# Kernel tuning notes

Hardware: AMD Instinct MI355X
Metric: run time of the kernel (lower is better)

## Reference

```python
import jax, jax.numpy as jnp
import numpy as np

NUM_HEADS = 16
CHUNK = 512


def setup_inputs() -> dict:
    key = jax.random.key(0)
    k1, k2, k3 = jax.random.split(key, 3)
    B, S, H = 2, 2048, 1024
    x = jax.random.normal(k1, (B, S, H), dtype=jnp.float32)
    w_qkv = jax.random.normal(k2, (H, 3 * H), dtype=jnp.float32) * 0.02
    b_qkv = jnp.zeros((3 * H,), dtype=jnp.float32)
    w_proj = jax.random.normal(k3, (H, H), dtype=jnp.float32) * 0.02
    b_proj = jnp.zeros((H,), dtype=jnp.float32)
    return {"x": x, "w_qkv": w_qkv, "b_qkv": b_qkv, "w_proj": w_proj, "b_proj": b_proj}


def reference(x, w_qkv, b_qkv, w_proj, b_proj):
    B, S, H = x.shape
    nh, cs = NUM_HEADS, CHUNK
    hd = H // nh
    nc = S // cs  # number of chunks (seq_len > chunk_size -> chunked branch)

    qkv = x @ w_qkv + b_qkv  # [B,S,3H]
    qkv = qkv.reshape(B, S, 3, nh, hd).transpose(2, 0, 3, 1, 4)  # [3,B,nh,S,hd]
    q, k, v = qkv[0], qkv[1], qkv[2]  # each [B,nh,S,hd]

    # split sequence into chunks: [B,nh,nc,cs,hd]
    qc = q.reshape(B, nh, nc, cs, hd)
    kc = k.reshape(B, nh, nc, cs, hd)
    vc = v.reshape(B, nh, nc, cs, hd)

    scale = 1.0 / jnp.sqrt(jnp.asarray(hd, dtype=x.dtype))
    # scores for every (q-chunk i, k-chunk j) pair: [B,nh,i,j,cs,cs]
    scores = jnp.einsum('bhicd,bhjed->bhijce', qc, kc) * scale
    # softmax is LOCAL to each k-chunk (per pair), matching the torch code
    attn = jax.nn.softmax(scores, axis=-1)
    # attend within each pair, then AVERAGE over k-chunks j
    out = jnp.einsum('bhijce,bhjed->bhicd', attn, vc) / nc  # [B,nh,nc,cs,hd]

    out = out.reshape(B, nh, S, hd).transpose(0, 2, 1, 3).reshape(B, S, H)
    # dropout is identity in eval mode
    return out @ w_proj + b_proj
```

## Files before the change

kernel.cpp:

```cpp
#include <hip/hip_runtime.h>
#include <hip/hip_bf16.h>
#include <stdint.h>

typedef __bf16 bf16;
typedef __bf16 bf16x8 __attribute__((ext_vector_type(8)));
typedef __bf16 bf16x4 __attribute__((ext_vector_type(4)));
typedef float f32x4 __attribute__((ext_vector_type(4)));

#define MFMA16(a, b, c) __builtin_amdgcn_mfma_f32_16x16x32_bf16(a, b, c, 0, 0, 0)
#define SBAR() __builtin_amdgcn_sched_barrier(0)

__device__ __forceinline__ void gload_lds16(const void* g, void* l) {
  __builtin_amdgcn_global_load_lds(
      (const __attribute__((address_space(1))) void*)g,
      (__attribute__((address_space(3))) void*)l, 16, 0, 0);
}


__global__ void prep_kernel(const float* __restrict__ x, bf16* __restrict__ xb,
                            const float* __restrict__ w_qkv,
                            bf16* __restrict__ wqkvT,
                            const float* __restrict__ w_proj,
                            bf16* __restrict__ wprojT) {
  __shared__ float t[32][65];
  const int bid = blockIdx.x;
  if (bid < 4096) {
    const int i = (bid * 256 + threadIdx.x) * 4;
    const float4 v = *(const float4*)(x + i);
    bf16x4 o = {(bf16)v.x, (bf16)v.y, (bf16)v.z, (bf16)v.w};
    *(bf16x4*)(xb + i) = o;
  } else {
    const float* in;
    bf16* out;
    int C, tile;
    if (bid < 5632) {
      in = w_qkv; out = wqkvT; C = 3072; tile = bid - 4096;
    } else {
      in = w_proj; out = wprojT; C = 1024; tile = bid - 5632;
    }
    const int ntx = C >> 5;
    const int c0 = (tile % ntx) * 32, r0 = (tile / ntx) * 64;
    const int tx = threadIdx.x & 31, ty = threadIdx.x >> 5;
#pragma unroll
    for (int i = 0; i < 64; i += 8)
      t[tx][ty + i] = in[(size_t)(r0 + ty + i) * C + c0 + tx];
    __syncthreads();
    const int orr = threadIdx.x & 63, oc4 = threadIdx.x >> 6;
#pragma unroll
    for (int i = 0; i < 32; i += 4) {
      const int oc = i + oc4;
      out[(size_t)(c0 + oc) * 1024 + r0 + orr] = (bf16)t[oc][orr];
    }
  }
}

__global__ void reduce_ctx(const bf16* __restrict__ p1, bf16* __restrict__ ctx) {
  const int i = (blockIdx.x * blockDim.x + threadIdx.x) * 8;
  const bf16x8 a = *(const bf16x8*)(ctx + i);
  const bf16x8 b = *(const bf16x8*)(p1 + i);
  bf16x8 o;
#pragma unroll
  for (int j = 0; j < 8; ++j)
    o[j] = (bf16)(0.25f * ((float)a[j] + (float)b[j]));
  *(bf16x8*)(ctx + i) = o;
}


__global__ __launch_bounds__(256, 2) void gemm_qkv(
    const bf16* __restrict__ A, const bf16* __restrict__ Bt,
    const float* __restrict__ bias, bf16* __restrict__ qp,
    bf16* __restrict__ kp, bf16* __restrict__ vT) {
  __shared__ __align__(16) char smem[65536];
  const int tid = threadIdx.x;
  const int wid = tid >> 6, lane = tid & 63;
  const int l15 = lane & 15, g = lane >> 4;
  const int wg = (blockIdx.x & 7) * 96 + (blockIdx.x >> 3);
  const int m0 = (wg / 24) * 128, n0 = (wg % 24) * 128;
  const int wr = wid >> 1, wc = wid & 1;
  const int K = 1024, nt = 16;

  const int srow8 = lane >> 3;
  const int sxor = ((lane & 7) ^ srow8) << 3;

  auto stage = [&](int t, int buf) {
    const int kt = t * 64;
    char* bufA = smem + buf * 32768;
    char* bufB = bufA + 16384;
#pragma unroll
    for (int c = 0; c < 4; ++c) {
      const int r = wid * 32 + c * 8 + srow8;
      gload_lds16(A + (size_t)(m0 + r) * K + kt + sxor,
                  bufA + wid * 4096 + c * 1024);
      gload_lds16(Bt + (size_t)(n0 + r) * K + kt + sxor,
                  bufB + wid * 4096 + c * 1024);
    }
  };

  f32x4 acc[4][4] = {};

  stage(0, 0);

  const int rsw = (l15 & 7) << 4;

#pragma unroll 1
  for (int t = 0; t < nt; ++t) {
    __syncthreads();
    SBAR();
    if (t + 1 < nt) stage(t + 1, (t + 1) & 1);
    const char* lA = smem + (t & 1) * 32768;
    const char* lB = lA + 16384;
#pragma unroll
    for (int kk = 0; kk < 2; ++kk) {
      const int kb = kk * 64 + g * 16;
      bf16x8 af[4], bfr[4];
#pragma unroll
      for (int mi = 0; mi < 4; ++mi)
        af[mi] = *(const bf16x8*)(lA + (wr * 64 + mi * 16 + l15) * 128 +
                                  (kb ^ rsw));
#pragma unroll
      for (int ni = 0; ni < 4; ++ni)
        bfr[ni] = *(const bf16x8*)(lB + (wc * 64 + ni * 16 + l15) * 128 +
                                   (kb ^ rsw));
      __builtin_amdgcn_s_setprio(1);
#pragma unroll
      for (int mi = 0; mi < 4; ++mi)
#pragma unroll
        for (int ni = 0; ni < 4; ++ni)
          acc[mi][ni] = MFMA16(af[mi], bfr[ni], acc[mi][ni]);
      __builtin_amdgcn_s_setprio(0);
    }
  }

  __syncthreads();
  const int b = m0 >> 11;
  if (n0 >= 2048) {
    bf16* T = (bf16*)smem + (size_t)wid * (64 * 68);
#pragma unroll
    for (int ni = 0; ni < 4; ++ni) {
      const float bv = bias[n0 + wc * 64 + ni * 16 + l15];
#pragma unroll
      for (int mi = 0; mi < 4; ++mi)
#pragma unroll
        for (int rg = 0; rg < 4; ++rg)
          T[(ni * 16 + l15) * 68 + mi * 16 + g * 4 + rg] =
              (bf16)(acc[mi][ni][rg] + bv);
    }
    const int hh = (n0 - 2048 + wc * 64) >> 6;
    const int sbase = (m0 & 2047) + wr * 64;
    const int l15p = (l15 & 8) | ((l15 & 3) << 1) | ((l15 >> 2) & 1);
    bf16* vrow = vT + ((size_t)(b * 16 + hh) * 64) * 2048 + sbase;
#pragma unroll
    for (int rr = 0; rr < 16; ++rr) {
      const int d = rr * 4 + g;
      const bf16x4 v4 = *(const bf16x4*)(T + d * 68 + l15 * 4);
      *(bf16x4*)(vrow + (size_t)d * 2048 + l15p * 4) = v4;
    }
  } else {
    const int sec = n0 >> 10;
    bf16* dst = (sec == 0) ? qp : kp;
    const float qscale = (sec == 0) ? 0.1803368801f : 1.0f;
#pragma unroll
    for (int mi = 0; mi < 4; ++mi) {
      const int rbase = m0 + wr * 64 + mi * 16 + g * 4;
#pragma unroll
      for (int ni = 0; ni < 4; ++ni) {
        const int cc = n0 + wc * 64 + ni * 16 + l15;
        const float bv = bias[cc];
        const int hh = (cc >> 6) & 15, d = cc & 63;
#pragma unroll
        for (int rg = 0; rg < 4; ++rg) {
          const int r = rbase + rg;
          const int s = r & 2047;
          dst[((size_t)(b * 16 + hh) * 2048 + s) * 64 + d] =
              (bf16)((acc[mi][ni][rg] + bv) * qscale);
        }
      }
    }
  }
}


__global__ __launch_bounds__(256, 2) void gemm_proj(
    const bf16* __restrict__ A, const bf16* __restrict__ Bt,
    const float* __restrict__ bias, float* __restrict__ Cout, int M, int N,
    int K, int nxb) {
  __shared__ __align__(16) char smem[65536];
  const int tid = threadIdx.x;
  const int wid = tid >> 6, lane = tid & 63;
  const int l15 = lane & 15, g = lane >> 4;
  const int cpx = gridDim.x >> 3;
  const int wg = (blockIdx.x & 7) * cpx + (blockIdx.x >> 3);
  const int m0 = (wg / nxb) * 128, n0 = (wg % nxb) * 128;
  const int wr = wid >> 1, wc = wid & 1;
  const int nt = K / 64;

  const int srow8 = lane >> 3;
  const int sxor = ((lane & 7) ^ srow8) << 3;

  auto stage = [&](int t, int buf) {
    const int kt = t * 64;
    char* bufA = smem + buf * 32768;
    char* bufB = bufA + 16384;
#pragma unroll
    for (int c = 0; c < 4; ++c) {
      const int r = wid * 32 + c * 8 + srow8;
      gload_lds16(A + (size_t)(m0 + r) * K + kt + sxor,
                  bufA + wid * 4096 + c * 1024);
      gload_lds16(Bt + (size_t)(n0 + r) * K + kt + sxor,
                  bufB + wid * 4096 + c * 1024);
    }
  };

  f32x4 acc[4][4] = {};

  stage(0, 0);

  const int rsw = (l15 & 7) << 4;

#pragma unroll 1
  for (int t = 0; t < nt; ++t) {
    __syncthreads();
    SBAR();
    if (t + 1 < nt) stage(t + 1, (t + 1) & 1);
    const char* lA = smem + (t & 1) * 32768;
    const char* lB = lA + 16384;
#pragma unroll
    for (int kk = 0; kk < 2; ++kk) {
      const int kb = kk * 64 + g * 16;
      bf16x8 af[4], bfr[4];
#pragma unroll
      for (int mi = 0; mi < 4; ++mi)
        af[mi] = *(const bf16x8*)(lA + (wr * 64 + mi * 16 + l15) * 128 +
                                  (kb ^ rsw));
#pragma unroll
      for (int ni = 0; ni < 4; ++ni)
        bfr[ni] = *(const bf16x8*)(lB + (wc * 64 + ni * 16 + l15) * 128 +
                                   (kb ^ rsw));
      __builtin_amdgcn_s_setprio(1);
#pragma unroll
      for (int mi = 0; mi < 4; ++mi)
#pragma unroll
        for (int ni = 0; ni < 4; ++ni)
          acc[mi][ni] = MFMA16(af[mi], bfr[ni], acc[mi][ni]);
      __builtin_amdgcn_s_setprio(0);
    }
  }

#pragma unroll
  for (int mi = 0; mi < 4; ++mi) {
    const int rbase = m0 + wr * 64 + mi * 16 + g * 4;
#pragma unroll
    for (int ni = 0; ni < 4; ++ni) {
      const int cc = n0 + wc * 64 + ni * 16 + l15;
      const float bv = bias[cc];
#pragma unroll
      for (int rg = 0; rg < 4; ++rg)
        Cout[(size_t)(rbase + rg) * N + cc] = acc[mi][ni][rg] + bv;
    }
  }
}


__global__ __launch_bounds__(256, 4) void attn_kernel(
    const bf16* __restrict__ qp, const bf16* __restrict__ kp,
    const bf16* __restrict__ vT, bf16* __restrict__ p0,
    bf16* __restrict__ p1) {
  __shared__ __align__(16) char lds_raw[32768];

  const int tid = threadIdx.x;
  const int wid = tid >> 6, lane = tid & 63;
  const int l15 = lane & 15, g = lane >> 4;
  const int wg = (blockIdx.x & 7) * 128 + (blockIdx.x >> 3);
  const int ch = wg & 1, qt = (wg >> 1) & 15, bhh = wg >> 5;
  const int h = bhh & 15, b = bhh >> 4;
  const size_t bh = (size_t)bhh;
  const int rowbase = b * 2048 + qt * 128;

  const bf16* qptr = qp + (bh * 2048 + (size_t)qt * 128 + wid * 32) * 64;
  bf16x8 Qf[2][2];
#pragma unroll
  for (int m = 0; m < 2; ++m)
#pragma unroll
    for (int hf = 0; hf < 2; ++hf)
      Qf[m][hf] =
          *(const bf16x8*)(qptr + (size_t)(m * 16 + l15) * 64 + hf * 32 + g * 8);

  bf16x8 ones;
#pragma unroll
  for (int i = 0; i < 8; ++i) ones[i] = (bf16)1.0f;

  const bf16* kbase = kp + bh * 2048 * 64;
  const bf16* vbase = vT + bh * 64 * 2048;

  const int srow = lane >> 3;
  const int scol = 8 * ((lane & 7) ^ srow);
  char* ldsK = lds_raw;
  char* ldsV = lds_raw + 16384;

  auto stage = [&](int tile, int buf) {
    const int r0 = wid * 16 + srow;
    const bf16* ks = kbase + ((size_t)tile * 64 + r0) * 64 + scol;
    char* kd = ldsK + buf * 8192 + wid * 2048;
    gload_lds16(ks, kd);
    gload_lds16(ks + 8 * 64, kd + 1024);
    const bf16* vs = vbase + (size_t)r0 * 2048 + tile * 64 + scol;
    char* vd = ldsV + buf * 8192 + wid * 2048;
    gload_lds16(vs, vd);
    gload_lds16(vs + 8 * 2048, vd + 1024);
  };

  f32x4 Otot[2][4] = {};
  const int swz = (l15 & 7) << 4;

  stage(ch * 16, 0);

#pragma unroll 1
  for (int c2 = 0; c2 < 2; ++c2) {
    f32x4 Och[2][4] = {};
    f32x4 ssum[2] = {};
#pragma unroll 1
    for (int h8 = 0; h8 < 8; ++h8) {
      const int t = c2 * 8 + h8;
      __syncthreads();
      SBAR();
      stage(ch * 16 + ((t + 1) & 15), (t + 1) & 1);
      const char* Kt = ldsK + (t & 1) * 8192;
      const char* Vt = ldsV + (t & 1) * 8192;
#pragma unroll
      for (int kk2 = 0; kk2 < 2; ++kk2) {
        f32x4 sacc[2][2] = {};
        __builtin_amdgcn_s_setprio(1);
#pragma unroll
        for (int b2 = 0; b2 < 2; ++b2)
#pragma unroll
          for (int hf = 0; hf < 2; ++hf) {
            const bf16x8 kf =
                *(const bf16x8*)(Kt + ((kk2 * 2 + b2) * 16 + l15) * 128 +
                                 ((hf * 64 + g * 16) ^ swz));
            sacc[b2][0] = MFMA16(kf, Qf[0][hf], sacc[b2][0]);
            sacc[b2][1] = MFMA16(kf, Qf[1][hf], sacc[b2][1]);
          }
        __builtin_amdgcn_s_setprio(0);
        bf16x8 af[2];
#pragma unroll
        for (int m = 0; m < 2; ++m)
#pragma unroll
          for (int j = 0; j < 4; ++j) {
            af[m][j] = (bf16)__builtin_amdgcn_exp2f(sacc[0][m][j]);
            af[m][4 + j] = (bf16)__builtin_amdgcn_exp2f(sacc[1][m][j]);
          }
        __builtin_amdgcn_s_setprio(1);
#pragma unroll
        for (int n = 0; n < 4; ++n) {
          const bf16x8 vf = *(const bf16x8*)(Vt + (n * 16 + l15) * 128 +
                                             ((kk2 * 64 + g * 16) ^ swz));
          Och[0][n] = MFMA16(af[0], vf, Och[0][n]);
          Och[1][n] = MFMA16(af[1], vf, Och[1][n]);
        }
        ssum[0] = MFMA16(af[0], ones, ssum[0]);
        ssum[1] = MFMA16(af[1], ones, ssum[1]);
        __builtin_amdgcn_s_setprio(0);
      }
    }
#pragma unroll
    for (int m = 0; m < 2; ++m)
#pragma unroll
      for (int rg = 0; rg < 4; ++rg) {
        const float inv = __builtin_amdgcn_rcpf(ssum[m][rg]);
#pragma unroll
        for (int n = 0; n < 4; ++n) Otot[m][n][rg] += Och[m][n][rg] * inv;
      }
  }

  bf16* pc = ch ? p1 : p0;
#pragma unroll
  for (int m = 0; m < 2; ++m)
#pragma unroll
    for (int n = 0; n < 4; ++n)
#pragma unroll
      for (int rg = 0; rg < 4; ++rg) {
        const int r = rowbase + wid * 32 + m * 16 + g * 4 + rg;
        pc[(size_t)r * 1024 + h * 64 + n * 16 + l15] = (bf16)Otot[m][n][rg];
      }
}


extern "C" void kernel_launch(void* const* d_in, const int* in_sizes, int n_in,
                              void* d_out, int out_size, void* d_ws,
                              size_t ws_size, hipStream_t stream) {
  const float* x = (const float*)d_in[0];
  const float* w_qkv = (const float*)d_in[1];
  const float* b_qkv = (const float*)d_in[2];
  const float* w_proj = (const float*)d_in[3];
  const float* b_proj = (const float*)d_in[4];
  float* out = (float*)d_out;

  char* ws = (char*)d_ws;
  bf16* xb     = (bf16*)(ws);
  bf16* wqkvT  = (bf16*)(ws + (8u << 20));
  bf16* wprojT = (bf16*)(ws + (14u << 20));
  bf16* qp     = (bf16*)(ws + (16u << 20));
  bf16* kp     = (bf16*)(ws + (24u << 20));
  bf16* vT     = (bf16*)(ws + (32u << 20));
  bf16* ctx    = (bf16*)(ws + (40u << 20));

  hipLaunchKernelGGL(prep_kernel, dim3(6144), dim3(256), 0, stream, x, xb,
                     w_qkv, wqkvT, w_proj, wprojT);
  hipLaunchKernelGGL(gemm_qkv, dim3(768), dim3(256), 0, stream, xb, wqkvT,
                     b_qkv, qp, kp, vT);
  hipLaunchKernelGGL(attn_kernel, dim3(1024), dim3(256), 0, stream, qp, kp, vT,
                     ctx, xb);
  hipLaunchKernelGGL(reduce_ctx, dim3(2048), dim3(256), 0, stream, xb, ctx);
  hipLaunchKernelGGL(gemm_proj, dim3(8 * 32), dim3(256), 0, stream, ctx,
                     wprojT, b_proj, out, 4096, 1024, 1024, 8);
}
```

Baseline: 99.61 us.

## Triple-buffer A tiles and use partial vmcnt waits in QKV and proj GEMMs

Both GEMM kernels now keep three LDS buffers for the A operand and two for B. A is prefetched two k-steps ahead and B one step ahead. The full __syncthreads is replaced by an explicit s_waitcnt vmcnt(4) plus s_barrier, so the next tile's loads can stay in flight while the current one is consumed, which aims to hide more global-load latency. LDS use rises from 64KB to 80KB per block. With launch_bounds(256,2) that is 160KB per CU, which should still fit the MI355X's 160KB LDS, but leaves no headroom.

```diff
diff --git a/kernel.cpp b/kernel.cpp
--- a/kernel.cpp
+++ b/kernel.cpp
@@ -70,7 +70,7 @@
     const bf16* __restrict__ A, const bf16* __restrict__ Bt,
     const float* __restrict__ bias, bf16* __restrict__ qp,
     bf16* __restrict__ kp, bf16* __restrict__ vT) {
-  __shared__ __align__(16) char smem[65536];
+  __shared__ __align__(16) char smem[81920];
   const int tid = threadIdx.x;
   const int wid = tid >> 6, lane = tid & 63;
   const int l15 = lane & 15, g = lane >> 4;
@@ -82,15 +82,22 @@
   const int srow8 = lane >> 3;
   const int sxor = ((lane & 7) ^ srow8) << 3;
 
-  auto stage = [&](int t, int buf) {
+  auto stageA = [&](int t) {
+    char* bufA = smem + (t % 3) * 16384;
     const int kt = t * 64;
-    char* bufA = smem + buf * 32768;
-    char* bufB = bufA + 16384;
 #pragma unroll
     for (int c = 0; c < 4; ++c) {
       const int r = wid * 32 + c * 8 + srow8;
       gload_lds16(A + (size_t)(m0 + r) * K + kt + sxor,
                   bufA + wid * 4096 + c * 1024);
+    }
+  };
+  auto stageB = [&](int t) {
+    char* bufB = smem + 49152 + (t & 1) * 16384;
+    const int kt = t * 64;
+#pragma unroll
+    for (int c = 0; c < 4; ++c) {
+      const int r = wid * 32 + c * 8 + srow8;
       gload_lds16(Bt + (size_t)(n0 + r) * K + kt + sxor,
                   bufB + wid * 4096 + c * 1024);
     }
@@ -98,17 +105,24 @@
 
   f32x4 acc[4][4] = {};
 
-  stage(0, 0);
+  stageA(0);
+  stageB(0);
+  stageA(1);
 
   const int rsw = (l15 & 7) << 4;
 
 #pragma unroll 1
   for (int t = 0; t < nt; ++t) {
-    __syncthreads();
+    if (t < nt - 1)
+      asm volatile("s_waitcnt vmcnt(4) lgkmcnt(0)" ::: "memory");
+    else
+      asm volatile("s_waitcnt vmcnt(0) lgkmcnt(0)" ::: "memory");
+    __builtin_amdgcn_s_barrier();
     SBAR();
-    if (t + 1 < nt) stage(t + 1, (t + 1) & 1);
-    const char* lA = smem + (t & 1) * 32768;
-    const char* lB = lA + 16384;
+    if (t + 1 < nt) stageB(t + 1);
+    if (t + 2 < nt) stageA(t + 2);
+    const char* lA = smem + (t % 3) * 16384;
+    const char* lB = smem + 49152 + (t & 1) * 16384;
 #pragma unroll
     for (int kk = 0; kk < 2; ++kk) {
       const int kb = kk * 64 + g * 16;
@@ -184,7 +198,7 @@
     const bf16* __restrict__ A, const bf16* __restrict__ Bt,
     const float* __restrict__ bias, float* __restrict__ Cout, int M, int N,
     int K, int nxb) {
-  __shared__ __align__(16) char smem[65536];
+  __shared__ __align__(16) char smem[81920];
   const int tid = threadIdx.x;
   const int wid = tid >> 6, lane = tid & 63;
   const int l15 = lane & 15, g = lane >> 4;
@@ -197,15 +211,22 @@
   const int srow8 = lane >> 3;
   const int sxor = ((lane & 7) ^ srow8) << 3;
 
-  auto stage = [&](int t, int buf) {
+  auto stageA = [&](int t) {
+    char* bufA = smem + (t % 3) * 16384;
     const int kt = t * 64;
-    char* bufA = smem + buf * 32768;
-    char* bufB = bufA + 16384;
 #pragma unroll
     for (int c = 0; c < 4; ++c) {
       const int r = wid * 32 + c * 8 + srow8;
       gload_lds16(A + (size_t)(m0 + r) * K + kt + sxor,
                   bufA + wid * 4096 + c * 1024);
+    }
+  };
+  auto stageB = [&](int t) {
+    char* bufB = smem + 49152 + (t & 1) * 16384;
+    const int kt = t * 64;
+#pragma unroll
+    for (int c = 0; c < 4; ++c) {
+      const int r = wid * 32 + c * 8 + srow8;
       gload_lds16(Bt + (size_t)(n0 + r) * K + kt + sxor,
                   bufB + wid * 4096 + c * 1024);
     }
@@ -213,17 +234,24 @@
 
   f32x4 acc[4][4] = {};
 
-  stage(0, 0);
+  stageA(0);
+  stageB(0);
+  stageA(1);
 
   const int rsw = (l15 & 7) << 4;
 
 #pragma unroll 1
   for (int t = 0; t < nt; ++t) {
-    __syncthreads();
+    if (t < nt - 1)
+      asm volatile("s_waitcnt vmcnt(4) lgkmcnt(0)" ::: "memory");
+    else
+      asm volatile("s_waitcnt vmcnt(0) lgkmcnt(0)" ::: "memory");
+    __builtin_amdgcn_s_barrier();
     SBAR();
-    if (t + 1 < nt) stage(t + 1, (t + 1) & 1);
-    const char* lA = smem + (t & 1) * 32768;
-    const char* lB = lA + 16384;
+    if (t + 1 < nt) stageB(t + 1);
+    if (t + 2 < nt) stageA(t + 2);
+    const char* lA = smem + (t % 3) * 16384;
+    const char* lB = smem + 49152 + (t & 1) * 16384;
 #pragma unroll
     for (int kk = 0; kk < 2; ++kk) {
       const int kb = kk * 64 + g * 16;
```

After: 101.0 us. Within noise of the previous version (+1.4%).
